# Kernel optimization log

Measured on AMD Instinct MI355X. Metric: run time of the kernel, lower is better.

## Reference

```python
import jax, jax.numpy as jnp
import numpy as np

B, T, E, H, G = 8, 1024, 1024, 16, 4
D = E // H
SCALING = D ** -0.5
READER_W = 0.1  # reader_group_weight


def _heads(x):
    # [B, T, E] -> [B, H, T, D]
    return x.reshape(B, T, H, D).transpose(0, 2, 1, 3)


def setup_inputs() -> dict:
    key = jax.random.key(0)
    ks = jax.random.split(key, 16)
    s = 0.02
    return {
        "hidden_states": jax.random.normal(ks[0], (B, T, E), jnp.float32),
        "reader_token": jax.random.randint(ks[1], (B,), 0, G, dtype=jnp.int32),
        # shared (generic) projections, torch Linear convention: y = x @ W.T + b
        "Wq": jax.random.normal(ks[2], (E, E), jnp.float32) * s,
        "bq": jnp.zeros((E,), jnp.float32),
        "Wk": jax.random.normal(ks[3], (E, E), jnp.float32) * s,
        "bk": jnp.zeros((E,), jnp.float32),
        "Wv": jax.random.normal(ks[4], (E, E), jnp.float32) * s,
        "bv": jnp.zeros((E,), jnp.float32),
        "Wo": jax.random.normal(ks[5], (E, E), jnp.float32) * s,
        "bo": jnp.zeros((E,), jnp.float32),
        # stacked per-reader-group expert projections [G, E, E]
        "RWq": jax.random.normal(ks[6], (G, E, E), jnp.float32) * s,
        "Rbq": jnp.zeros((G, E), jnp.float32),
        "RWk": jax.random.normal(ks[7], (G, E, E), jnp.float32) * s,
        "Rbk": jnp.zeros((G, E), jnp.float32),
        "RWv": jax.random.normal(ks[8], (G, E, E), jnp.float32) * s,
        "Rbv": jnp.zeros((G, E), jnp.float32),
    }


def reference(hidden_states, reader_token, Wq, bq, Wk, bk, Wv, bv, Wo, bo,
              RWq, Rbq, RWk, Rbk, RWv, Rbv):
    hs = hidden_states
    # --- generic attention probs (shared weights) ---
    q = _heads((hs @ Wq.T + bq) * SCALING)          # [B,H,T,D]
    k = _heads(hs @ Wk.T + bk)                       # [B,H,T,D]
    v = _heads(hs @ Wv.T + bv)                       # [B,H,T,D]
    gen_probs = jax.nn.softmax(jnp.einsum('bhtd,bhsd->bhts', q, k), axis=-1)
    # --- reader-group attention probs (per-sample routed weights) ---
    Wq_b = RWq[reader_token]                          # [B,E,E]
    Wk_b = RWk[reader_token]
    q_r = _heads((jnp.einsum('bte,boe->bto', hs, Wq_b) + Rbq[reader_token][:, None, :]) * SCALING)
    k_r = _heads(jnp.einsum('bte,boe->bto', hs, Wk_b) + Rbk[reader_token][:, None, :])
    rdr_probs = jax.nn.softmax(jnp.einsum('bhtd,bhsd->bhts', q_r, k_r), axis=-1)
    # --- weighted combine, then attend over GENERIC value states ---
    probs = (READER_W * rdr_probs + (1.0 - READER_W) * gen_probs) / 2.0
    attn = jnp.einsum('bhts,bhsd->bhtd', probs, v)    # [B,H,T,D]
    attn = attn.transpose(0, 2, 1, 3).reshape(B, T, E)
    return attn @ Wo.T + bo
```

## Files before the change

### kernel.cpp

```cpp
#include <hip/hip_runtime.h>
#include <stdint.h>

#define AS1 __attribute__((address_space(1)))
#define AS3 __attribute__((address_space(3)))

typedef __attribute__((ext_vector_type(8))) short bf16x8;
typedef __attribute__((ext_vector_type(4))) float f32x4;

#define NB 8
#define NT 1024
#define NE 1024
#define NH 16
#define BT (NB * NT)

__device__ __forceinline__ unsigned short f2bf(float f) {
    unsigned int u = __builtin_bit_cast(unsigned int, f);
    u += 0x7FFFu + ((u >> 16) & 1u);
    return (unsigned short)(u >> 16);
}
__device__ __forceinline__ unsigned int cvt_pk_bf16(float lo, float hi) {
    unsigned int r;
    asm("v_cvt_pk_bf16_f32 %0, %1, %2" : "=v"(r) : "v"(lo), "v"(hi));
    return r;
}

__global__ void k_cvt7(const float* __restrict__ hs, unsigned short* __restrict__ hsB,
                       const float* __restrict__ w1, unsigned short* __restrict__ w1B,
                       const float* __restrict__ w2, unsigned short* __restrict__ w2B,
                       const float* __restrict__ w3, unsigned short* __restrict__ w3B,
                       const float* __restrict__ w4, unsigned short* __restrict__ w4B,
                       const float* __restrict__ r1, unsigned short* __restrict__ r1B,
                       const float* __restrict__ r2, unsigned short* __restrict__ r2B)
{
    int blk = blockIdx.x;
    const float* s; unsigned short* d; int base;
    if      (blk < 8192)  { s = hs; d = hsB; base = 0; }
    else if (blk < 9216)  { s = w1; d = w1B; base = 8192; }
    else if (blk < 10240) { s = w2; d = w2B; base = 9216; }
    else if (blk < 11264) { s = w3; d = w3B; base = 10240; }
    else if (blk < 12288) { s = w4; d = w4B; base = 11264; }
    else if (blk < 16384) { s = r1; d = r1B; base = 12288; }
    else                  { s = r2; d = r2B; base = 16384; }
    int i = ((blk - base) * 256 + threadIdx.x) * 4;
    float4 f = *reinterpret_cast<const float4*>(s + i);
    ushort4 o;
    o.x = f2bf(f.x); o.y = f2bf(f.y); o.z = f2bf(f.z); o.w = f2bf(f.w);
    *reinterpret_cast<ushort4*>(d + i) = o;
}

struct GJob {
    const unsigned short* W;
    const float* bias;
    void* out;
    float scale;
    int routed;
};

template <bool OUT_F32>
__global__ __launch_bounds__(512, 1)
void k_gemmN(const unsigned short* __restrict__ A,
             GJob j0, GJob j1, GJob j2, GJob j3, GJob j4,
             const int* __restrict__ rt)
{
    __shared__ __attribute__((aligned(16))) unsigned short LA[3][2][128 * 64];
    __shared__ __attribute__((aligned(16))) unsigned short LBb[3][128 * 64];

    const int flat = blockIdx.x;
    const int xcd = flat & 7;
    const int l   = flat >> 3;
    const int pz  = l >> 5;
    const int r   = l & 31;
    const int by  = xcd * 4 + (r >> 3);
    const int bx  = r & 7;
    const int m0 = by << 8, n0 = bx << 7;

    GJob jb = j0;
    if (pz == 1) jb = j1;
    else if (pz == 2) jb = j2;
    else if (pz == 3) jb = j3;
    else if (pz == 4) jb = j4;
    int g = jb.routed ? rt[m0 >> 10] : 0;
    const unsigned short* Wg = jb.W + (size_t)g * NE * NE;

    const int tid  = threadIdx.x;
    const int wid  = tid >> 6;
    const int lane = tid & 63;
    const int frow = lane & 15;
    const int g4   = lane >> 4;
    const int wm = wid >> 1, wn = wid & 1;

    const int rh0  = tid >> 3;
    const int swz8 = ((tid & 7) ^ (rh0 & 7)) * 8;
    const unsigned short* baseA = A  + (size_t)m0 * NE;
    const unsigned short* baseB = Wg + (size_t)n0 * NE;

    auto STAGE_A = [&](int d, int half, int kt) {
#pragma unroll
        for (int j = 0; j < 2; ++j) {
            const unsigned short* src =
                baseA + (size_t)(half * 128 + rh0 + j * 64) * NE + kt * 64 + swz8;
            __builtin_amdgcn_global_load_lds((AS1 void*)src,
                (AS3 void*)&LA[d][half][(tid + j * 512) * 8], 16, 0, 0);
        }
    };
    auto STAGE_B = [&](int d, int kt) {
#pragma unroll
        for (int j = 0; j < 2; ++j) {
            const unsigned short* src =
                baseB + (size_t)(rh0 + j * 64) * NE + kt * 64 + swz8;
            __builtin_amdgcn_global_load_lds((AS1 void*)src,
                (AS3 void*)&LBb[d][(tid + j * 512) * 8], 16, 0, 0);
        }
    };

    f32x4 acc[4][4];
#pragma unroll
    for (int m = 0; m < 4; ++m)
#pragma unroll
        for (int n = 0; n < 4; ++n) acc[m][n] = (f32x4){0.f, 0.f, 0.f, 0.f};

    bf16x8 a4[4], b4[4];
    auto RDA = [&](int d, int kh) {
#pragma unroll
        for (int mf = 0; mf < 4; ++mf) {
            int rowin = (wm & 1) * 64 + mf * 16 + frow;
            int off = rowin * 64 + (((kh * 4 + g4) ^ (frow & 7)) * 8);
            a4[mf] = *reinterpret_cast<const bf16x8*>(&LA[d][wm >> 1][off]);
        }
    };
    auto RDB = [&](int d, int kh) {
#pragma unroll
        for (int nf = 0; nf < 4; ++nf) {
            int rowin = wn * 64 + nf * 16 + frow;
            int off = rowin * 64 + (((kh * 4 + g4) ^ (frow & 7)) * 8);
            b4[nf] = *reinterpret_cast<const bf16x8*>(&LBb[d][off]);
        }
    };
    auto MM = [&]() {
        __builtin_amdgcn_s_setprio(1);
#pragma unroll
        for (int mf = 0; mf < 4; ++mf)
#pragma unroll
            for (int nf = 0; nf < 4; ++nf)
                acc[mf][nf] =
                    __builtin_amdgcn_mfma_f32_16x16x32_bf16(a4[mf], b4[nf], acc[mf][nf], 0, 0, 0);
        __builtin_amdgcn_s_setprio(0);
    };

#define BARX __builtin_amdgcn_s_barrier()
#define LGK0 asm volatile("s_waitcnt lgkmcnt(0)" ::: "memory")
#define VMC6 asm volatile("s_waitcnt vmcnt(6)" ::: "memory")
#define VMC0 asm volatile("s_waitcnt vmcnt(0)" ::: "memory")

    STAGE_A(0, 0, 0); STAGE_A(0, 1, 0); STAGE_B(0, 0);
    STAGE_A(1, 0, 1); STAGE_A(1, 1, 1); STAGE_B(1, 1);
    VMC6; BARX;

    int bt = 0;
#pragma unroll 1
    for (int t = 0; t < 16; ++t) {
        const int b2 = (bt + 2 >= 3) ? bt - 1 : bt + 2;
        const bool pre = (t + 2 < 16);
        RDA(bt, 0); RDB(bt, 0);
        if (pre) STAGE_A(b2, 0, t + 2);
        BARX; LGK0; MM(); BARX;
        RDA(bt, 1); RDB(bt, 1);
        if (pre) { STAGE_A(b2, 1, t + 2); STAGE_B(b2, t + 2); }
        BARX; LGK0; MM();
        if (t < 14) { VMC6; } else if (t == 14) { VMC0; }
        BARX;
        bt = (bt + 1 >= 3) ? 0 : bt + 1;
    }
#undef BARX
#undef LGK0
#undef VMC6
#undef VMC0

    const float* biasg = jb.bias + (size_t)g * NE;
#pragma unroll
    for (int am = 0; am < 4; ++am) {
        int row = m0 + wm * 64 + am * 16 + g4 * 4;
#pragma unroll
        for (int nf = 0; nf < 4; ++nf) {
            int col = n0 + wn * 64 + nf * 16 + frow;
            float bv = biasg[col];
            f32x4 v = acc[am][nf];
#pragma unroll
            for (int r2 = 0; r2 < 4; ++r2) {
                float val = (v[r2] + bv) * jb.scale;
                if (OUT_F32)
                    ((float*)jb.out)[(size_t)(row + r2) * NE + col] = val;
                else
                    ((unsigned short*)jb.out)[(size_t)(row + r2) * NE + col] = f2bf(val);
            }
        }
    }
}

__global__ void k_vtrans(const unsigned short* __restrict__ V, unsigned short* __restrict__ Vt) {
    __shared__ unsigned short tile[64][65];
    const int blk = blockIdx.x;
    const int bh = blk >> 4;
    const int b = bh >> 4;
    const int h = bh & 15;
    const int s0 = (blk & 15) * 64;
    const int tid = threadIdx.x;
#pragma unroll
    for (int i = 0; i < 2; ++i) {
        int seg = tid + i * 256;
        int row = seg >> 3;
        int c8 = (seg & 7) * 8;
        const unsigned short* src = V + (size_t)(b * NT + s0 + row) * NE + h * 64 + c8;
        ushort4 u0 = *reinterpret_cast<const ushort4*>(src);
        ushort4 u1 = *reinterpret_cast<const ushort4*>(src + 4);
        tile[row][c8 + 0] = u0.x; tile[row][c8 + 1] = u0.y;
        tile[row][c8 + 2] = u0.z; tile[row][c8 + 3] = u0.w;
        tile[row][c8 + 4] = u1.x; tile[row][c8 + 5] = u1.y;
        tile[row][c8 + 6] = u1.z; tile[row][c8 + 7] = u1.w;
    }
    __syncthreads();
#pragma unroll
    for (int i = 0; i < 2; ++i) {
        int seg = tid + i * 256;
        int drow = seg >> 3;
        int s8 = (seg & 7) * 8;
        ushort4 u0, u1;
        u0.x = tile[s8 + 0][drow]; u0.y = tile[s8 + 1][drow];
        u0.z = tile[s8 + 2][drow]; u0.w = tile[s8 + 3][drow];
        u1.x = tile[s8 + 4][drow]; u1.y = tile[s8 + 5][drow];
        u1.z = tile[s8 + 6][drow]; u1.w = tile[s8 + 7][drow];
        unsigned short* dst = Vt + (size_t)(bh * 64 + drow) * NT + s0 + s8;
        *reinterpret_cast<ushort4*>(dst) = u0;
        *reinterpret_cast<ushort4*>(dst + 4) = u1;
    }
}

__global__ __launch_bounds__(512, 4)
void k_attn(const unsigned short* __restrict__ Q,
            const unsigned short* __restrict__ K,
            const unsigned short* __restrict__ Qr,
            const unsigned short* __restrict__ Kr,
            const unsigned short* __restrict__ Vt,
            unsigned short* __restrict__ attnO)
{
    constexpr int PLD = 40;
    __shared__ __attribute__((aligned(16))) unsigned short KV[2][3 * 4096];
    __shared__ __attribute__((aligned(16))) unsigned short Pga[8][16 * PLD];
    __shared__ __attribute__((aligned(16))) unsigned short Pra[8][16 * PLD];

    const int blk = (blockIdx.x & 7) * 128 + (blockIdx.x >> 3);
    const int tile = blk & 7;
    const int bh = blk >> 3;
    const int b = bh >> 4;
    const int h = bh & 15;
    const int wid = threadIdx.x >> 6;
    const int lane = threadIdx.x & 63;
    const int frow = lane & 15;
    const int g4 = lane >> 4;
    const int f7 = frow & 7;
    const int fk8 = g4 * 8;
    const int t0 = tile * 128 + wid * 16;

    const size_t qoff = (size_t)(b * NT + t0 + frow) * NE + h * 64;
    const bf16x8 qf0 = *reinterpret_cast<const bf16x8*>(Q + qoff + fk8);
    const bf16x8 qf1 = *reinterpret_cast<const bf16x8*>(Q + qoff + 32 + fk8);
    const bf16x8 qr0 = *reinterpret_cast<const bf16x8*>(Qr + qoff + fk8);
    const bf16x8 qr1 = *reinterpret_cast<const bf16x8*>(Qr + qoff + 32 + fk8);

    const unsigned short* Kb  = K  + (size_t)b * NT * NE + h * 64;
    const unsigned short* Krb = Kr + (size_t)b * NT * NE + h * 64;
    const unsigned short* Vtb = Vt + (size_t)bh * 64 * NT;
    unsigned short* PgRow = &Pga[wid][0] + frow * PLD;
    unsigned short* PrRow = &Pra[wid][0] + frow * PLD;

    f32x4 og[4], orr[4];
    float lgp = 0.f, lrp = 0.f;
#pragma unroll
    for (int i = 0; i < 4; ++i) {
        og[i] = (f32x4){0.f, 0.f, 0.f, 0.f};
        orr[i] = (f32x4){0.f, 0.f, 0.f, 0.f};
    }

    const int srow = threadIdx.x >> 3;
    const int scb8 = ((threadIdx.x & 7) ^ (srow & 7)) * 8;
    auto stage = [&](int buf, int s0) {
        const unsigned short* sK = Kb  + (size_t)(s0 + srow) * NE + scb8;
        const unsigned short* sR = Krb + (size_t)(s0 + srow) * NE + scb8;
        const unsigned short* sV = Vtb + (size_t)srow * NT + s0 + scb8;
        __builtin_amdgcn_global_load_lds((AS1 void*)sK, (AS3 void*)(&KV[buf][wid * 512]), 16, 0, 0);
        __builtin_amdgcn_global_load_lds((AS1 void*)sR, (AS3 void*)(&KV[buf][4096 + wid * 512]), 16, 0, 0);
        __builtin_amdgcn_global_load_lds((AS1 void*)sV, (AS3 void*)(&KV[buf][8192 + wid * 512]), 16, 0, 0);
    };

    stage(0, 0);
    __syncthreads();
    int cur = 0;
    const f32x4 z = (f32x4){0.f, 0.f, 0.f, 0.f};
#pragma unroll 1
    for (int t = 0; t < NT / 64; ++t) {
        if (t < NT / 64 - 1) stage(cur ^ 1, (t + 1) * 64);
        const unsigned short* Kl  = &KV[cur][0];
        const unsigned short* Krl = &KV[cur][4096];
        const unsigned short* Vl  = &KV[cur][8192];

        f32x4 sg[4], sr[4];
#pragma unroll
        for (int nf = 0; nf < 4; ++nf) {
            const int ro = (nf * 16 + frow) * 64;
            bf16x8 kA = *reinterpret_cast<const bf16x8*>(Kl + ro + ((g4 ^ f7) * 8));
            bf16x8 kB = *reinterpret_cast<const bf16x8*>(Kl + ro + (((4 + g4) ^ f7) * 8));
            bf16x8 rA = *reinterpret_cast<const bf16x8*>(Krl + ro + ((g4 ^ f7) * 8));
            bf16x8 rB = *reinterpret_cast<const bf16x8*>(Krl + ro + (((4 + g4) ^ f7) * 8));
            sg[nf] = __builtin_amdgcn_mfma_f32_16x16x32_bf16(kA, qf0, z, 0, 0, 0);
            sg[nf] = __builtin_amdgcn_mfma_f32_16x16x32_bf16(kB, qf1, sg[nf], 0, 0, 0);
            sr[nf] = __builtin_amdgcn_mfma_f32_16x16x32_bf16(rA, qr0, z, 0, 0, 0);
            sr[nf] = __builtin_amdgcn_mfma_f32_16x16x32_bf16(rB, qr1, sr[nf], 0, 0, 0);
        }

#pragma unroll
        for (int hh = 0; hh < 2; ++hh) {
#pragma unroll
            for (int j = 0; j < 2; ++j) {
                const int nf = 2 * hh + j;
                float g0 = __expf(sg[nf][0]), g1 = __expf(sg[nf][1]);
                float g2 = __expf(sg[nf][2]), g3 = __expf(sg[nf][3]);
                lgp += (g0 + g1) + (g2 + g3);
                uint2 wg;
                wg.x = cvt_pk_bf16(g0, g1);
                wg.y = cvt_pk_bf16(g2, g3);
                *reinterpret_cast<uint2*>(PgRow + j * 16 + g4 * 4) = wg;
                float r0 = __expf(sr[nf][0]), r1 = __expf(sr[nf][1]);
                float r2 = __expf(sr[nf][2]), r3 = __expf(sr[nf][3]);
                lrp += (r0 + r1) + (r2 + r3);
                uint2 wr;
                wr.x = cvt_pk_bf16(r0, r1);
                wr.y = cvt_pk_bf16(r2, r3);
                *reinterpret_cast<uint2*>(PrRow + j * 16 + g4 * 4) = wr;
            }
            asm volatile("s_waitcnt lgkmcnt(0)" ::: "memory");
            bf16x8 pg = *reinterpret_cast<const bf16x8*>(PgRow + fk8);
            bf16x8 pr = *reinterpret_cast<const bf16x8*>(PrRow + fk8);
            __builtin_amdgcn_s_setprio(1);
#pragma unroll
            for (int nf2 = 0; nf2 < 4; ++nf2) {
                const int vo = (nf2 * 16 + frow) * 64;
                bf16x8 v = *reinterpret_cast<const bf16x8*>(Vl + vo + (((4 * hh + g4) ^ f7) * 8));
                og[nf2]  = __builtin_amdgcn_mfma_f32_16x16x32_bf16(pg, v, og[nf2], 0, 0, 0);
                orr[nf2] = __builtin_amdgcn_mfma_f32_16x16x32_bf16(pr, v, orr[nf2], 0, 0, 0);
            }
            __builtin_amdgcn_s_setprio(0);
        }

        __syncthreads();
        cur ^= 1;
    }

    lgp += __shfl_xor(lgp, 16); lgp += __shfl_xor(lgp, 32);
    lrp += __shfl_xor(lrp, 16); lrp += __shfl_xor(lrp, 32);
    float ig = 0.45f / lgp, ir = 0.05f / lrp;
    float igr[4], irr[4];
#pragma unroll
    for (int r = 0; r < 4; ++r) {
        igr[r] = __shfl(ig, g4 * 4 + r);
        irr[r] = __shfl(ir, g4 * 4 + r);
    }
#pragma unroll
    for (int nf2 = 0; nf2 < 4; ++nf2) {
#pragma unroll
        for (int r = 0; r < 4; ++r) {
            float val = og[nf2][r] * igr[r] + orr[nf2][r] * irr[r];
            int tq = t0 + g4 * 4 + r;
            attnO[(size_t)(b * NT + tq) * NE + h * 64 + nf2 * 16 + frow] = f2bf(val);
        }
    }
}

extern "C" void kernel_launch(void* const* d_in, const int* in_sizes, int n_in,
                              void* d_out, int out_size, void* d_ws, size_t ws_size,
                              hipStream_t stream)
{
    const float* hs  = (const float*)d_in[0];
    const int*   rt  = (const int*)d_in[1];
    const float* Wq  = (const float*)d_in[2];
    const float* bq  = (const float*)d_in[3];
    const float* Wk  = (const float*)d_in[4];
    const float* bk  = (const float*)d_in[5];
    const float* Wv  = (const float*)d_in[6];
    const float* bv  = (const float*)d_in[7];
    const float* Wo  = (const float*)d_in[8];
    const float* bo  = (const float*)d_in[9];
    const float* RWq = (const float*)d_in[10];
    const float* Rbq = (const float*)d_in[11];
    const float* RWk = (const float*)d_in[12];
    const float* Rbk = (const float*)d_in[13];

    unsigned short* w = (unsigned short*)d_ws;
    const size_t NBT = (size_t)BT * NE;
    const size_t NW  = (size_t)NE * NE;
    unsigned short* hsB  = w; w += NBT;
    unsigned short* Qb   = w; w += NBT;
    unsigned short* Kb   = w; w += NBT;
    unsigned short* Vb   = w; w += NBT;
    unsigned short* Qrb  = w; w += NBT;
    unsigned short* Krb  = w; w += NBT;
    unsigned short* Vtb  = w; w += NBT;
    unsigned short* atb  = w; w += NBT;
    unsigned short* WqB  = w; w += NW;
    unsigned short* WkB  = w; w += NW;
    unsigned short* WvB  = w; w += NW;
    unsigned short* WoB  = w; w += NW;
    unsigned short* RWqB = w; w += 4 * NW;
    unsigned short* RWkB = w; w += 4 * NW;

    k_cvt7<<<dim3(20480), dim3(256), 0, stream>>>(hs, hsB, Wq, WqB, Wk, WkB, Wv, WvB,
                                                  Wo, WoB, RWq, RWqB, RWk, RWkB);

    GJob jq  = { WqB,  bq,  Qb,  0.125f, 0 };
    GJob jk  = { WkB,  bk,  Kb,  1.0f,   0 };
    GJob jv  = { WvB,  bv,  Vb,  1.0f,   0 };
    GJob jrq = { RWqB, Rbq, Qrb, 0.125f, 1 };
    GJob jrk = { RWkB, Rbk, Krb, 1.0f,   1 };
    k_gemmN<false><<<dim3(1280), dim3(512), 0, stream>>>(hsB, jq, jk, jv, jrq, jrk, rt);

    k_vtrans<<<dim3(NB * NH * 16), dim3(256), 0, stream>>>(Vb, Vtb);
    k_attn<<<dim3(NB * NH * 8), dim3(512), 0, stream>>>(Qb, Kb, Qrb, Krb, Vtb, atb);

    GJob jo = { WoB, bo, d_out, 1.0f, 0 };
    k_gemmN<true><<<dim3(256), dim3(512), 0, stream>>>(atb, jo, jo, jo, jo, jo, nullptr);
}
```

Measured before the change: 240.9 us.

## Replace QKV projection GEMM with 256x256-tile pipelined kernel

Adds a new projection GEMM kernel that uses 256x256 output tiles instead of 256x128. It double-buffers A and B halves in LDS with direct global-to-LDS loads, and interleaves staging with MFMA phases under fine-grained barriers. Larger tiles raise arithmetic intensity and halve the grid to 640 blocks. In exchange it needs more accumulator registers, targets 2 blocks per CU, and the finer schedule adds many barriers.

Result: faster. 232.3 us, median of 2 (-3.6%).

```diff
diff --git a/kernel.cpp b/kernel.cpp
--- a/kernel.cpp
+++ b/kernel.cpp
@@ -57,6 +57,142 @@
 };
 
 template <bool OUT_F32>
+__global__ __launch_bounds__(512, 2)
+void k_gemm256(const unsigned short* __restrict__ A,
+               GJob j0, GJob j1, GJob j2, GJob j3, GJob j4,
+               const int* __restrict__ rt)
+{
+    __shared__ __attribute__((aligned(16))) unsigned short LB[2][2][2][128 * 64];
+
+    const int flat = blockIdx.x;
+    const int xcd = flat & 7;
+    const int l   = flat >> 3;
+    const int pz  = l >> 4;
+    const int r   = l & 15;
+    const int by  = xcd * 4 + (r >> 2);
+    const int bx  = r & 3;
+    const int m0 = by << 8, n0 = bx << 8;
+
+    GJob jb = j0;
+    if (pz == 1) jb = j1;
+    else if (pz == 2) jb = j2;
+    else if (pz == 3) jb = j3;
+    else if (pz == 4) jb = j4;
+    int g = jb.routed ? rt[m0 >> 10] : 0;
+    const unsigned short* Wg = jb.W + (size_t)g * NE * NE;
+
+    const int tid  = threadIdx.x;
+    const int wid  = tid >> 6;
+    const int lane = tid & 63;
+    const int frow = lane & 15;
+    const int g4   = lane >> 4;
+    const int wm = wid >> 2, wn = wid & 3;
+
+    const int rh0  = tid >> 3;
+    const int swz8 = ((tid & 7) ^ (rh0 & 7)) * 8;
+    const unsigned short* baseA = A  + (size_t)m0 * NE;
+    const unsigned short* baseB = Wg + (size_t)n0 * NE;
+
+    auto STAGE = [&](int d, int mat, int half, int kt) {
+        const unsigned short* base = mat ? baseB : baseA;
+#pragma unroll
+        for (int j = 0; j < 2; ++j) {
+            const unsigned short* src =
+                base + (size_t)(half * 128 + rh0 + j * 64) * NE + kt * 64 + swz8;
+            __builtin_amdgcn_global_load_lds((AS1 void*)src,
+                (AS3 void*)&LB[d][mat][half][(wid * 64 + j * 512) * 8], 16, 0, 0);
+        }
+    };
+
+    f32x4 acc[8][4];
+#pragma unroll
+    for (int m = 0; m < 8; ++m)
+#pragma unroll
+        for (int n = 0; n < 4; ++n) acc[m][n] = (f32x4){0.f, 0.f, 0.f, 0.f};
+
+    bf16x8 a4[4], b4[4];
+    auto RDA = [&](int d, int mh, int kh) {
+#pragma unroll
+        for (int mf = 0; mf < 4; ++mf) {
+            int rh = mh * 64 + mf * 16 + frow;
+            int off = rh * 64 + (((kh * 4 + g4) ^ (frow & 7)) * 8);
+            a4[mf] = *reinterpret_cast<const bf16x8*>(&LB[d][0][wm][off]);
+        }
+    };
+    auto RDB = [&](int d, int kh) {
+#pragma unroll
+        for (int nf = 0; nf < 4; ++nf) {
+            int rh = (wn & 1) * 64 + nf * 16 + frow;
+            int off = rh * 64 + (((kh * 4 + g4) ^ (frow & 7)) * 8);
+            b4[nf] = *reinterpret_cast<const bf16x8*>(&LB[d][1][wn >> 1][off]);
+        }
+    };
+    auto MM = [&](int mh) {
+        __builtin_amdgcn_s_setprio(1);
+#pragma unroll
+        for (int mf = 0; mf < 4; ++mf)
+#pragma unroll
+            for (int nf = 0; nf < 4; ++nf)
+                acc[mh * 4 + mf][nf] =
+                    __builtin_amdgcn_mfma_f32_16x16x32_bf16(a4[mf], b4[nf], acc[mh * 4 + mf][nf], 0, 0, 0);
+        __builtin_amdgcn_s_setprio(0);
+    };
+
+#define BARX __builtin_amdgcn_s_barrier()
+#define LGK0 asm volatile("s_waitcnt lgkmcnt(0)" ::: "memory")
+#define VMC2 asm volatile("s_waitcnt vmcnt(2)" ::: "memory")
+
+    STAGE(0, 0, 0, 0); STAGE(0, 0, 1, 0); STAGE(0, 1, 0, 0); STAGE(0, 1, 1, 0);
+    STAGE(1, 1, 0, 1);
+    VMC2; BARX;
+
+#pragma unroll 1
+    for (int i = 0; i < 8; ++i) {
+        const int t = 2 * i;
+        const bool pre = (i < 7);
+        RDA(0, 0, 0); RDB(0, 0); STAGE(1, 1, 1, t + 1);
+        BARX; LGK0; MM(0); BARX;
+        RDA(0, 1, 0); STAGE(1, 0, 0, t + 1);
+        BARX; LGK0; MM(1); BARX;
+        RDA(0, 0, 1); RDB(0, 1); STAGE(1, 0, 1, t + 1);
+        BARX; LGK0; MM(0); BARX;
+        RDA(0, 1, 1); if (pre) STAGE(0, 1, 0, t + 2);
+        BARX; LGK0; MM(1); VMC2; BARX;
+        RDA(1, 0, 0); RDB(1, 0); if (pre) STAGE(0, 1, 1, t + 2);
+        BARX; LGK0; MM(0); BARX;
+        RDA(1, 1, 0); if (pre) STAGE(0, 0, 0, t + 2);
+        BARX; LGK0; MM(1); BARX;
+        RDA(1, 0, 1); RDB(1, 1); if (pre) STAGE(0, 0, 1, t + 2);
+        BARX; LGK0; MM(0); BARX;
+        RDA(1, 1, 1); if (pre) STAGE(1, 1, 0, t + 3);
+        BARX; LGK0; MM(1); VMC2; BARX;
+    }
+#undef BARX
+#undef LGK0
+#undef VMC2
+
+    const float* biasg = jb.bias + (size_t)(jb.routed ? (rt[m0 >> 10]) : 0) * NE;
+#pragma unroll
+    for (int am = 0; am < 8; ++am) {
+        int row = m0 + wm * 128 + am * 16 + g4 * 4;
+#pragma unroll
+        for (int nf = 0; nf < 4; ++nf) {
+            int col = n0 + wn * 64 + nf * 16 + frow;
+            float bv = biasg[col];
+            f32x4 v = acc[am][nf];
+#pragma unroll
+            for (int r2 = 0; r2 < 4; ++r2) {
+                float val = (v[r2] + bv) * jb.scale;
+                if (OUT_F32)
+                    ((float*)jb.out)[(size_t)(row + r2) * NE + col] = val;
+                else
+                    ((unsigned short*)jb.out)[(size_t)(row + r2) * NE + col] = f2bf(val);
+            }
+        }
+    }
+}
+
+template <bool OUT_F32>
 __global__ __launch_bounds__(512, 1)
 void k_gemmN(const unsigned short* __restrict__ A,
              GJob j0, GJob j1, GJob j2, GJob j3, GJob j4,
@@ -420,7 +556,7 @@
     GJob jv  = { WvB,  bv,  Vb,  1.0f,   0 };
     GJob jrq = { RWqB, Rbq, Qrb, 0.125f, 1 };
     GJob jrk = { RWkB, Rbk, Krb, 1.0f,   1 };
-    k_gemmN<false><<<dim3(1280), dim3(512), 0, stream>>>(hsB, jq, jk, jv, jrq, jrk, rt);
+    k_gemm256<false><<<dim3(640), dim3(512), 0, stream>>>(hsB, jq, jk, jv, jrq, jrk, rt);
 
     k_vtrans<<<dim3(NB * NH * 16), dim3(256), 0, stream>>>(Vb, Vtb);
     k_attn<<<dim3(NB * NH * 8), dim3(512), 0, stream>>>(Qb, Kb, Qrb, Krb, Vtb, atb);
```
